# Kernel tuning notes

Hardware: AMD Instinct MI355X
Metric: run time of the kernel (lower is better)

The kernel has to match this reference:

```python
import jax, jax.numpy as jnp
import numpy as np

H = 256
LATENT = 128
NODE_FEATS = (12, 5, 4)
EDGE_FEATS = (5, 4)
END_NODE = NODE_FEATS[0] - 1
MAX_NODES = 64


def setup_inputs() -> dict:
    key = jax.random.key(0)
    ks = iter(jax.random.split(key, 40))
    def rn(shape, s=0.1):
        return jax.random.normal(next(ks), shape, dtype=jnp.float32) * s
    inp = {
        "z": jax.random.normal(next(ks), (1, LATENT), dtype=jnp.float32),
        "lp_w": rn((H, LATENT)), "lp_b": rn((H,)),
        "nWih": rn((3 * H, H)), "nWhh": rn((3 * H, H)), "nbih": rn((3 * H,)), "nbhh": rn((3 * H,)),
        "eWih": rn((3 * H, H)), "eWhh": rn((3 * H, H)), "ebih": rn((3 * H,)), "ebhh": rn((3 * H,)),
    }
    for j, f in enumerate(NODE_FEATS):
        inp[f"nc{j}_w"] = rn((f, H)); inp[f"nc{j}_b"] = rn((f,))
    for j, f in enumerate(EDGE_FEATS):
        inp[f"ec{j}_w"] = rn((f, H)); inp[f"ec{j}_b"] = rn((f,))
    inp["max_nodes"] = MAX_NODES
    return inp


def _gru(x, h, Wih, Whh, bih, bhh):
    # torch.nn.GRU single step, single layer. x,h: (1,H)
    gi = x @ Wih.T + bih
    gh = h @ Whh.T + bhh
    ir, iz, inn = jnp.split(gi, 3, axis=-1)
    hr, hz, hn = jnp.split(gh, 3, axis=-1)
    r = jax.nn.sigmoid(ir + hr)
    zg = jax.nn.sigmoid(iz + hz)
    n = jnp.tanh(inn + r * hn)
    return (1.0 - zg) * n + zg * h


def _classify(emb, W, b):
    # Linear -> softmax -> (max prob, argmax), batch=1 -> scalars
    p = jax.nn.softmax(emb @ W.T + b, axis=-1)[0]
    return jnp.max(p), jnp.argmax(p)


def _generate(z, lp_w, lp_b, nWih, nWhh, nbih, nbhh, eWih, eWhh, ebih, ebhh,
              nc0_w, nc0_b, nc1_w, nc1_b, nc2_w, nc2_b,
              ec0_w, ec0_b, ec1_w, ec1_b, max_nodes):
    node_cls = ((nc0_w, nc0_b), (nc1_w, nc1_b), (nc2_w, nc2_b))
    edge_cls = ((ec0_w, ec0_b), (ec1_w, ec1_b))
    h0 = z @ lp_w.T + lp_b                     # latent_project; set_context
    buf0 = jnp.zeros((max_nodes, 1, H), z.dtype)  # node embedding history

    def step(carry, i):
        h, buf, done = carry
        x = jnp.where(i == 0, jnp.zeros((1, H), z.dtype), buf[jnp.maximum(i - 1, 0)])
        h1 = _gru(x, h, nWih, nWhh, nbih, nbhh)   # node_celli.forward_unit; emb = h1
        nps, nis = zip(*[_classify(h1, W, b) for W, b in node_cls])
        nprobs = jnp.stack(nps)                   # (3,)
        nidxs = jnp.stack(nis)                    # (3,) int
        is_end = nidxs[0] == END_NODE

        # edge cell: seq over previous node embeddings, most recent first
        def estep(he, t):
            valid = t < i
            src = jnp.clip(i - 1 - t, 0, max_nodes - 1)
            he2 = _gru(buf[src], he, eWih, eWhh, ebih, ebhh)
            he_new = jnp.where(valid, he2, he)
            eps, eis = zip(*[_classify(he_new, W, b) for W, b in edge_cls])
            return he_new, (jnp.stack(eps), jnp.stack(eis))

        he_fin, (ep_t, ei_t) = jax.lax.scan(estep, h1, jnp.arange(max_nodes))
        # reindex: edge for source node j was produced at inner step t = i-1-j
        js = jnp.arange(max_nodes)
        ts = jnp.clip(i - 1 - js, 0, max_nodes - 1)
        ep_row = ep_t[ts]                          # (max_nodes, 2)
        ei_row = ei_t[ts]
        vj = js < i
        no_edges = jnp.all(jnp.where(vj, ei_row[:, 0] == 0, True)) & (i > 0)

        active = jnp.logical_not(done)
        node_ok = active & jnp.logical_not(is_end) & jnp.logical_not(no_edges)
        done_new = done | is_end | no_edges

        h_next = jnp.where(node_ok & (i > 0), he_fin, h1)  # node hidden <- edge hidden
        h_next = jnp.where(active, h_next, h)
        buf_new = buf.at[i].set(jnp.where(node_ok, h1, buf[i]))

        edge_valid = vj & node_ok & (i > 0)
        out = (jnp.where(node_ok, nprobs, 0.0), nidxs, node_ok,
               jnp.where(edge_valid[:, None], ep_row, 0.0), ei_row, edge_valid)
        return (h_next, buf_new, done_new), out

    _, outs = jax.lax.scan(step, (h0, buf0, jnp.zeros((), bool)), jnp.arange(max_nodes))
    # node_probs (M,3), node_idxs (M,3), node_valid (M,),
    # edge_probs (M,M,2), edge_idxs (M,M,2), edge_valid (M,M)
    return outs


def reference(z, lp_w, lp_b, nWih, nWhh, nbih, nbhh, eWih, eWhh, ebih, ebhh,
              nc0_w, nc0_b, nc1_w, nc1_b, nc2_w, nc2_b,
              ec0_w, ec0_b, ec1_w, ec1_b, max_nodes):
    return _generate(z, lp_w, lp_b, nWih, nWhh, nbih, nbhh, eWih, eWhh, ebih, ebhh,
                     nc0_w, nc0_b, nc1_w, nc1_b, nc2_w, nc2_b,
                     ec0_w, ec0_b, ec1_w, ec1_b, max_nodes)
```

## Files before the change

### kernel.cpp

```cpp
#include <hip/hip_runtime.h>
#include <stdint.h>


#define H 256
#define HL 128
#define G3 768
#define NW 16
#define SL 16
#define MAXN 64
#define NSTATE (1 + MAXN + (MAXN*(MAXN-1))/2)
#define SENTU 0xFFFFFFFFu
#define PAD 264

#define WG_CLS NW
#define WG_HELP0 (NW+1)
#define NHELP_PER 6
#define NROLE (WG_HELP0 + 2*NHELP_PER)
#define NWG 256

#define NP_OFF 0
#define NI_OFF 192
#define NV_OFF 384
#define EP_OFF 448
#define EI_OFF (EP_OFF + MAXN*MAXN*2)
#define EV_OFF (EI_OFF + MAXN*MAXN*2)

struct Wksp {
  float h[NSTATE][H];
  float gi_e[MAXN][G3];
  float gi_n[MAXN][G3];
  unsigned int dec[MAXN];
};

union Shm {
  struct {
    float whe[3*SL*PAD];
    float whn[3*SL*PAD];
    float hcur[2][H];
    float bihe[3*SL], bhhe[3*SL], bihn[3*SL], bhhn[3*SL];
    float zv[HL];
    unsigned int dec;
  } w;
  struct {
    float cw[30*H];
    float cb[30];
    float hc[H];
    float logits[30];
    float resp[5];
    int   resi[5];
    float ept[MAXN][2];
    int   eit[MAXN][2];
  } c;
  struct { float h1[H]; } hp;
};

__device__ __forceinline__ float spinf(const float* p) {
  const unsigned int* u = (const unsigned int*)p;
  unsigned int v = __hip_atomic_load(u, __ATOMIC_RELAXED, __HIP_MEMORY_SCOPE_AGENT);
  while (v == SENTU)
    v = __hip_atomic_load(u, __ATOMIC_RELAXED, __HIP_MEMORY_SCOPE_AGENT);
  return __uint_as_float(v);
}
__device__ __forceinline__ void pubf(float* p, float x) {
  __hip_atomic_store((unsigned int*)p, __float_as_uint(x),
                     __ATOMIC_RELAXED, __HIP_MEMORY_SCOPE_AGENT);
}
__device__ __forceinline__ unsigned int spinu(const unsigned int* p) {
  unsigned int v = __hip_atomic_load(p, __ATOMIC_RELAXED, __HIP_MEMORY_SCOPE_AGENT);
  while (v == SENTU)
    v = __hip_atomic_load(p, __ATOMIC_RELAXED, __HIP_MEMORY_SCOPE_AGENT);
  return v;
}
__device__ __forceinline__ void pubu(unsigned int* p, unsigned int x) {
  __hip_atomic_store(p, x, __ATOMIC_RELAXED, __HIP_MEMORY_SCOPE_AGENT);
}
__device__ __forceinline__ float sigm(float x) { return 1.0f / (1.0f + expf(-x)); }

__global__ __launch_bounds__(256)
void Generator_34746285425383_kernel(
    const float* __restrict__ z, const float* __restrict__ lp_w, const float* __restrict__ lp_b,
    const float* __restrict__ nWih, const float* __restrict__ nWhh,
    const float* __restrict__ nbih, const float* __restrict__ nbhh,
    const float* __restrict__ eWih, const float* __restrict__ eWhh,
    const float* __restrict__ ebih, const float* __restrict__ ebhh,
    const float* __restrict__ nc0w, const float* __restrict__ nc0b,
    const float* __restrict__ nc1w, const float* __restrict__ nc1b,
    const float* __restrict__ nc2w, const float* __restrict__ nc2b,
    const float* __restrict__ ec0w, const float* __restrict__ ec0b,
    const float* __restrict__ ec1w, const float* __restrict__ ec1b,
    float* __restrict__ out, Wksp* __restrict__ ws)
{
  __shared__ Shm S;
  const int bid = blockIdx.x;
  const int tid = threadIdx.x;

  if (bid < NW) {
    const int w = bid, g = tid >> 4, c = tid & 15;
    const int k = w * SL + g;
    for (int r = 0; r < 3 * SL; ++r) {
      const int gate = r / SL, gg = r % SL;
      const int grow = gate * H + (w * SL + gg);
      for (int col = tid; col < H; col += 256) {
        S.w.whe[r * PAD + col] = eWhh[grow * H + col];
        S.w.whn[r * PAD + col] = nWhh[grow * H + col];
      }
    }
    if (tid < 3 * SL) {
      const int gate = tid / SL, gg = tid % SL;
      const int grow = gate * H + w * SL + gg;
      S.w.bihe[tid] = ebih[grow]; S.w.bhhe[tid] = ebhh[grow];
      S.w.bihn[tid] = nbih[grow]; S.w.bhhn[tid] = nbhh[grow];
    }
    if (tid < HL) S.w.zv[tid] = z[tid];
    __syncthreads();

    {
      float p = 0.f;
      for (int it = 0; it < 8; ++it) {
        const int col = c + 16 * it;
        p += S.w.zv[col] * lp_w[k * HL + col];
      }
      for (int off = 1; off < 16; off <<= 1) p += __shfl_xor(p, off);
      if (c == 0) pubf(&ws->h[0][k], p + lp_b[k]);
    }

    int m = 1, idx_carry = 0;
    bool done = false;
    unsigned long long valid = 0ull;
    float pg0 = 0.f, pg1 = 0.f, pg2 = 0.f;
    const float* pga = nullptr;

    for (int i = 0; i < MAXN; ++i) {
      for (int t = -1; t < i; ++t) {
        const bool is_node = (t < 0);
        const int hidx = is_node ? idx_carry : (m - 1);
        const int src  = is_node ? (i - 1) : (i - 1 - t);
        float* hc = S.w.hcur[m & 1];
        hc[tid] = spinf(&ws->h[hidx][tid]);
        float gi0 = 0.f, gi1 = 0.f, gi2 = 0.f;
        const bool use_gi = (src >= 0) && ((valid >> src) & 1ull);
        if (use_gi) {
          gi0 = pg0; gi1 = pg1; gi2 = pg2;
          if (__float_as_uint(gi0) == SENTU) gi0 = spinf(&pga[0 * H + k]);
          if (__float_as_uint(gi1) == SENTU) gi1 = spinf(&pga[1 * H + k]);
          if (__float_as_uint(gi2) == SENTU) gi2 = spinf(&pga[2 * H + k]);
        }
        __syncthreads();
        const float* Wl = is_node ? S.w.whn : S.w.whe;
        float p0 = 0.f, p1 = 0.f, p2 = 0.f;
        #pragma unroll
        for (int it = 0; it < 16; ++it) {
          const int col = c + 16 * it;
          const float hv = hc[col];
          p0 += Wl[(0 * SL + g) * PAD + col] * hv;
          p1 += Wl[(1 * SL + g) * PAD + col] * hv;
          p2 += Wl[(2 * SL + g) * PAD + col] * hv;
        }
        for (int off = 1; off < 16; off <<= 1) {
          p0 += __shfl_xor(p0, off);
          p1 += __shfl_xor(p1, off);
          p2 += __shfl_xor(p2, off);
        }
        const float* bih = is_node ? S.w.bihn : S.w.bihe;
        const float* bhh = is_node ? S.w.bhhn : S.w.bhhe;
        const float rr = sigm(gi0 + bih[0 * SL + g] + p0 + bhh[0 * SL + g]);
        const float zz = sigm(gi1 + bih[1 * SL + g] + p1 + bhh[1 * SL + g]);
        const float nn = tanhf(gi2 + bih[2 * SL + g] + rr * (p2 + bhh[2 * SL + g]));
        const float hp = (1.f - zz) * nn + zz * hc[k];
        if (c == 0) pubf(&ws->h[m][k], hp);
        {
          int ni = i, nt = t + 1;
          if (nt >= i) { ni = i + 1; nt = -1; }
          if (ni < MAXN) {
            const bool nnode = (nt < 0);
            const int nsrc = nnode ? (ni - 1) : (ni - 1 - nt);
            if (nsrc >= 0) {
              pga = nnode ? ws->gi_n[nsrc] : ws->gi_e[nsrc];
              pg0 = __builtin_nontemporal_load(&pga[0 * H + k]);
              pg1 = __builtin_nontemporal_load(&pga[1 * H + k]);
              pg2 = __builtin_nontemporal_load(&pga[2 * H + k]);
            }
          }
        }
        ++m;
      }
      if (tid == 0) S.w.dec = spinu(&ws->dec[i]);
      __syncthreads();
      const unsigned int dec = S.w.dec;
      const bool is_end   = (dec >> 1) & 1u;
      const bool no_edges = (dec >> 2) & 1u;
      const bool active   = !done;
      const bool node_ok  = active && !is_end && !no_edges;
      if (node_ok) valid |= (1ull << i);
      const int s_end = m - 1, node_m = m - 1 - i;
      if (active) idx_carry = (node_ok && i > 0) ? s_end : node_m;
      done = done || is_end || no_edges;
    }

  } else if (bid == WG_CLS) {
    const int g = tid >> 4, c = tid & 15;
    const float* wsrc[5] = { nc0w, nc1w, nc2w, ec0w, ec1w };
    const float* bsrc[5] = { nc0b, nc1b, nc2b, ec0b, ec1b };
    const int hbase[5] = { 0, 12, 17, 21, 26 };
    const int hlen[5]  = { 12, 5, 4, 5, 4 };
    for (int hh = 0; hh < 5; ++hh)
      for (int r = 0; r < hlen[hh]; ++r)
        for (int col = tid; col < H; col += 256)
          S.c.cw[(hbase[hh] + r) * H + col] = wsrc[hh][r * H + col];
    if (tid < 30) {
      const int hh = tid < 12 ? 0 : tid < 17 ? 1 : tid < 21 ? 2 : tid < 26 ? 3 : 4;
      S.c.cb[tid] = bsrc[hh][tid - hbase[hh]];
    }
    __syncthreads();

    int m = 1;
    bool done = false;
    for (int i = 0; i < MAXN; ++i) {
      float npmax[3]; int nidx[3];
      bool is_end = false, andacc = true;
      for (int t = -1; t < i; ++t) {
        S.c.hc[tid] = spinf(&ws->h[m][tid]);
        __syncthreads();
        for (int rsel = 0; rsel < 2; ++rsel) {
          const int r = g + 16 * rsel;
          float p = 0.f;
          if (r < 30) {
            #pragma unroll
            for (int it = 0; it < 16; ++it) {
              const int col = c + 16 * it;
              p += S.c.cw[r * H + col] * S.c.hc[col];
            }
          }
          for (int off = 1; off < 16; off <<= 1) p += __shfl_xor(p, off);
          if (r < 30 && c == 0) S.c.logits[r] = p + S.c.cb[r];
        }
        __syncthreads();
        if (tid < 5) {
          const int base = hbase[tid], len = hlen[tid];
          float best = S.c.logits[base]; int bi = 0;
          for (int j = 1; j < len; ++j) {
            const float l = S.c.logits[base + j];
            if (l > best) { best = l; bi = j; }
          }
          float s = 0.f;
          for (int j = 0; j < len; ++j) s += expf(S.c.logits[base + j] - best);
          S.c.resp[tid] = 1.0f / s;
          S.c.resi[tid] = bi;
        }
        __syncthreads();
        if (t < 0) {
          npmax[0] = S.c.resp[0]; npmax[1] = S.c.resp[1]; npmax[2] = S.c.resp[2];
          nidx[0] = S.c.resi[0]; nidx[1] = S.c.resi[1]; nidx[2] = S.c.resi[2];
          is_end = (S.c.resi[0] == 11);
          if (i == 0 && tid == 0) {
            S.c.ept[0][0] = S.c.resp[3]; S.c.ept[0][1] = S.c.resp[4];
            S.c.eit[0][0] = S.c.resi[3]; S.c.eit[0][1] = S.c.resi[4];
          }
        } else {
          if (tid == 0) {
            S.c.ept[t][0] = S.c.resp[3]; S.c.ept[t][1] = S.c.resp[4];
            S.c.eit[t][0] = S.c.resi[3]; S.c.eit[t][1] = S.c.resi[4];
          }
          andacc = andacc && (S.c.resi[3] == 0);
        }
        __syncthreads();
        ++m;
      }
      const bool no_edges = (i > 0) && andacc;
      const bool active = !done;
      const bool node_ok = active && !is_end && !no_edges;
      if (tid == 0)
        pubu(&ws->dec[i], 1u | (is_end ? 2u : 0u) | (no_edges ? 4u : 0u));
      if (tid < MAXN) {
        const int j = tid;
        const bool vj = j < i;
        const bool ev = vj && node_ok && (i > 0);
        const int tt = vj ? (i - 1 - j) : 0;
        out[EP_OFF + (i * MAXN + j) * 2 + 0] = ev ? S.c.ept[tt][0] : 0.f;
        out[EP_OFF + (i * MAXN + j) * 2 + 1] = ev ? S.c.ept[tt][1] : 0.f;
        out[EI_OFF + (i * MAXN + j) * 2 + 0] = (float)S.c.eit[tt][0];
        out[EI_OFF + (i * MAXN + j) * 2 + 1] = (float)S.c.eit[tt][1];
        out[EV_OFF + i * MAXN + j] = ev ? 1.f : 0.f;
      } else if (tid < MAXN + 8) {
        const int q = tid - MAXN;
        if (q < 3)       out[NP_OFF + i * 3 + q]       = node_ok ? npmax[q] : 0.f;
        else if (q < 6)  out[NI_OFF + i * 3 + (q - 3)] = (float)nidx[q - 3];
        else if (q == 6) out[NV_OFF + i]               = node_ok ? 1.f : 0.f;
      }
      done = done || is_end || no_edges;
      __syncthreads();
    }

  } else if (bid < NROLE) {
    const int e = bid - WG_HELP0;
    const bool is_edge = (e < NHELP_PER);
    const int rowbase = (e % NHELP_PER) * 128;
    const float* Wih = is_edge ? eWih : nWih;
    float* gdst = is_edge ? &ws->gi_e[0][0] : &ws->gi_n[0][0];
    const int g = tid >> 4, c = tid & 15;
    int m_node = 1;
    for (int i = 0; i < MAXN; ++i) {
      S.hp.h1[tid] = spinf(&ws->h[m_node][tid]);
      __syncthreads();
      for (int rr = 0; rr < 8; ++rr) {
        const int row = rowbase + g * 8 + rr;
        float p = 0.f;
        #pragma unroll
        for (int u = 0; u < 4; ++u) {
          const float4 wv = *(const float4*)&Wih[row * H + c * 16 + u * 4];
          p += wv.x * S.hp.h1[c * 16 + u * 4 + 0]
             + wv.y * S.hp.h1[c * 16 + u * 4 + 1]
             + wv.z * S.hp.h1[c * 16 + u * 4 + 2]
             + wv.w * S.hp.h1[c * 16 + u * 4 + 3];
        }
        for (int off = 1; off < 16; off <<= 1) p += __shfl_xor(p, off);
        if (c == 0) pubf(&gdst[i * G3 + row], p);
      }
      __syncthreads();
      m_node += 1 + i;
    }

  } else {
    const unsigned int* flag = &ws->dec[MAXN - 1];
    float acc = (float)tid * 0.001f;
    const float bb = 1.0000001f, aa = 0.5f;
    for (;;) {
      unsigned int v = __hip_atomic_load(flag, __ATOMIC_RELAXED, __HIP_MEMORY_SCOPE_AGENT);
      if (v != SENTU) break;
      #pragma unroll 8
      for (int it = 0; it < 512; ++it) acc = __builtin_fmaf(acc, bb, aa);
    }
    asm volatile("" :: "v"(acc));
  }
}

extern "C" void kernel_launch(void* const* d_in, const int* in_sizes, int n_in,
                              void* d_out, int out_size, void* d_ws, size_t ws_size,
                              hipStream_t stream) {
  hipMemsetAsync(d_ws, 0xFF, sizeof(Wksp), stream);
  Generator_34746285425383_kernel<<<dim3(NWG), dim3(256), 0, stream>>>(
      (const float*)d_in[0],  (const float*)d_in[1],  (const float*)d_in[2],
      (const float*)d_in[3],  (const float*)d_in[4],  (const float*)d_in[5],
      (const float*)d_in[6],  (const float*)d_in[7],  (const float*)d_in[8],
      (const float*)d_in[9],  (const float*)d_in[10],
      (const float*)d_in[11], (const float*)d_in[12],
      (const float*)d_in[13], (const float*)d_in[14],
      (const float*)d_in[15], (const float*)d_in[16],
      (const float*)d_in[17], (const float*)d_in[18],
      (const float*)d_in[19], (const float*)d_in[20],
      (float*)d_out, (Wksp*)d_ws);
}
```

Baseline: 5.079 ms.

## Co-locate all pipeline roles on one XCC and poll via L2-coherent sc0 loads

Each workgroup reads its XCC id and takes a per-XCC ticket. The first XCC to gather enough workgroups for every role becomes the winner, and roles are handed out only to workgroups on that XCC, so all cross-workgroup flag and data exchange stays within one XCD's L2. Publishes and polls add sc0 global loads and stores, with a bounded retry before falling back to agent-scope atomics. The spare spinning heater workgroups are removed, and a timeout path falls back to the original blockIdx-based role assignment. This adds a startup election, an extra memset, and reliance on per-XCC cache coherence behaviour.

```diff
diff --git a/kernel.cpp b/kernel.cpp
--- a/kernel.cpp
+++ b/kernel.cpp
@@ -1,5 +1,6 @@
 #include <hip/hip_runtime.h>
 #include <stdint.h>
+#include <cstddef>
 
 
 #define H 256
@@ -10,6 +11,7 @@
 #define MAXN 64
 #define NSTATE (1 + MAXN + (MAXN*(MAXN-1))/2)
 #define SENTU 0xFFFFFFFFu
+#define DEADV 0x0000DEADu
 #define PAD 264
 
 #define WG_CLS NW
@@ -30,6 +32,9 @@
   float gi_e[MAXN][G3];
   float gi_n[MAXN][G3];
   unsigned int dec[MAXN];
+  unsigned int winner;
+  unsigned int padw[7];
+  unsigned int ticket[8];
 };
 
 union Shm {
@@ -54,25 +59,37 @@
   struct { float h1[H]; } hp;
 };
 
-__device__ __forceinline__ float spinf(const float* p) {
-  const unsigned int* u = (const unsigned int*)p;
-  unsigned int v = __hip_atomic_load(u, __ATOMIC_RELAXED, __HIP_MEMORY_SCOPE_AGENT);
-  while (v == SENTU)
-    v = __hip_atomic_load(u, __ATOMIC_RELAXED, __HIP_MEMORY_SCOPE_AGENT);
-  return __uint_as_float(v);
+__device__ __forceinline__ unsigned int ld_sc0(const unsigned int* p) {
+  unsigned int v;
+  asm volatile("global_load_dword %0, %1, off sc0\n\ts_waitcnt vmcnt(0)"
+               : "=&v"(v) : "v"(p) : "memory");
+  return v;
+}
+__device__ __forceinline__ void st_sc0(unsigned int* p, unsigned int v) {
+  asm volatile("global_store_dword %0, %1, off sc0" :: "v"(p), "v"(v) : "memory");
+}
+__device__ __forceinline__ unsigned int ld_ag(const unsigned int* p) {
+  return __hip_atomic_load(p, __ATOMIC_RELAXED, __HIP_MEMORY_SCOPE_AGENT);
+}
+__device__ __forceinline__ void pub_u(unsigned int* p, unsigned int v) {
+  __hip_atomic_store(p, v, __ATOMIC_RELAXED, __HIP_MEMORY_SCOPE_AGENT);
+  st_sc0(p, v);
 }
 __device__ __forceinline__ void pubf(float* p, float x) {
-  __hip_atomic_store((unsigned int*)p, __float_as_uint(x),
-                     __ATOMIC_RELAXED, __HIP_MEMORY_SCOPE_AGENT);
-}
-__device__ __forceinline__ unsigned int spinu(const unsigned int* p) {
-  unsigned int v = __hip_atomic_load(p, __ATOMIC_RELAXED, __HIP_MEMORY_SCOPE_AGENT);
-  while (v == SENTU)
-    v = __hip_atomic_load(p, __ATOMIC_RELAXED, __HIP_MEMORY_SCOPE_AGENT);
+  pub_u((unsigned int*)p, __float_as_uint(x));
+}
+__device__ __forceinline__ unsigned int spin_u(const unsigned int* p, bool sc) {
+  unsigned int v;
+  if (sc) {
+    int tries = 0;
+    v = ld_sc0(p);
+    while (v == SENTU && ++tries < 8) v = ld_sc0(p);
+  } else v = ld_ag(p);
+  while (v == SENTU) v = ld_ag(p);
   return v;
 }
-__device__ __forceinline__ void pubu(unsigned int* p, unsigned int x) {
-  __hip_atomic_store(p, x, __ATOMIC_RELAXED, __HIP_MEMORY_SCOPE_AGENT);
+__device__ __forceinline__ float spinf(const float* p, bool sc) {
+  return __uint_as_float(spin_u((const unsigned int*)p, sc));
 }
 __device__ __forceinline__ float sigm(float x) { return 1.0f / (1.0f + expf(-x)); }
 
@@ -91,8 +108,43 @@
     float* __restrict__ out, Wksp* __restrict__ ws)
 {
   __shared__ Shm S;
-  const int bid = blockIdx.x;
+  __shared__ int role_s, mode_s;
   const int tid = threadIdx.x;
+
+  if (tid == 0) {
+    unsigned int xcc;
+    asm volatile("s_getreg_b32 %0, hwreg(HW_REG_XCC_ID)" : "=s"(xcc));
+    xcc &= 7u;
+    const unsigned int slot = __hip_atomic_fetch_add(&ws->ticket[xcc], 1u,
+                                __ATOMIC_RELAXED, __HIP_MEMORY_SCOPE_AGENT);
+    if (slot == NROLE - 1) {
+      unsigned int exp = SENTU;
+      __hip_atomic_compare_exchange_strong(&ws->winner, &exp, xcc,
+          __ATOMIC_RELAXED, __ATOMIC_RELAXED, __HIP_MEMORY_SCOPE_AGENT);
+    }
+    unsigned int wv = ld_ag(&ws->winner);
+    int iters = 0;
+    while (wv == SENTU) {
+      ++iters;
+      if (iters > 1500 && blockIdx.x == 0) {
+        unsigned int exp = SENTU;
+        __hip_atomic_compare_exchange_strong(&ws->winner, &exp, DEADV,
+            __ATOMIC_RELAXED, __ATOMIC_RELAXED, __HIP_MEMORY_SCOPE_AGENT);
+      }
+      wv = ld_ag(&ws->winner);
+    }
+    if (wv <= 7u) {
+      role_s = (wv == xcc && slot < NROLE) ? (int)slot : -1;
+      mode_s = 1;
+    } else {
+      role_s = ((int)blockIdx.x < NROLE) ? (int)blockIdx.x : -1;
+      mode_s = 0;
+    }
+  }
+  __syncthreads();
+  const int bid = role_s;
+  const bool sc = (mode_s != 0);
+  if (bid < 0) return;
 
   if (bid < NW) {
     const int w = bid, g = tid >> 4, c = tid & 15;
@@ -136,14 +188,14 @@
         const int hidx = is_node ? idx_carry : (m - 1);
         const int src  = is_node ? (i - 1) : (i - 1 - t);
         float* hc = S.w.hcur[m & 1];
-        hc[tid] = spinf(&ws->h[hidx][tid]);
+        hc[tid] = spinf(&ws->h[hidx][tid], sc);
         float gi0 = 0.f, gi1 = 0.f, gi2 = 0.f;
         const bool use_gi = (src >= 0) && ((valid >> src) & 1ull);
         if (use_gi) {
           gi0 = pg0; gi1 = pg1; gi2 = pg2;
-          if (__float_as_uint(gi0) == SENTU) gi0 = spinf(&pga[0 * H + k]);
-          if (__float_as_uint(gi1) == SENTU) gi1 = spinf(&pga[1 * H + k]);
-          if (__float_as_uint(gi2) == SENTU) gi2 = spinf(&pga[2 * H + k]);
+          if (__float_as_uint(gi0) == SENTU) gi0 = spinf(&pga[0 * H + k], sc);
+          if (__float_as_uint(gi1) == SENTU) gi1 = spinf(&pga[1 * H + k], sc);
+          if (__float_as_uint(gi2) == SENTU) gi2 = spinf(&pga[2 * H + k], sc);
         }
         __syncthreads();
         const float* Wl = is_node ? S.w.whn : S.w.whe;
@@ -184,7 +236,7 @@
         }
         ++m;
       }
-      if (tid == 0) S.w.dec = spinu(&ws->dec[i]);
+      if (tid == 0) S.w.dec = spin_u(&ws->dec[i], sc);
       __syncthreads();
       const unsigned int dec = S.w.dec;
       const bool is_end   = (dec >> 1) & 1u;
@@ -219,7 +271,7 @@
       float npmax[3]; int nidx[3];
       bool is_end = false, andacc = true;
       for (int t = -1; t < i; ++t) {
-        S.c.hc[tid] = spinf(&ws->h[m][tid]);
+        S.c.hc[tid] = spinf(&ws->h[m][tid], sc);
         __syncthreads();
         for (int rsel = 0; rsel < 2; ++rsel) {
           const int r = g + 16 * rsel;
@@ -270,7 +322,7 @@
       const bool active = !done;
       const bool node_ok = active && !is_end && !no_edges;
       if (tid == 0)
-        pubu(&ws->dec[i], 1u | (is_end ? 2u : 0u) | (no_edges ? 4u : 0u));
+        pub_u(&ws->dec[i], 1u | (is_end ? 2u : 0u) | (no_edges ? 4u : 0u));
       if (tid < MAXN) {
         const int j = tid;
         const bool vj = j < i;
@@ -291,7 +343,7 @@
       __syncthreads();
     }
 
-  } else if (bid < NROLE) {
+  } else {
     const int e = bid - WG_HELP0;
     const bool is_edge = (e < NHELP_PER);
     const int rowbase = (e % NHELP_PER) * 128;
@@ -300,7 +352,7 @@
     const int g = tid >> 4, c = tid & 15;
     int m_node = 1;
     for (int i = 0; i < MAXN; ++i) {
-      S.hp.h1[tid] = spinf(&ws->h[m_node][tid]);
+      S.hp.h1[tid] = spinf(&ws->h[m_node][tid], sc);
       __syncthreads();
       for (int rr = 0; rr < 8; ++rr) {
         const int row = rowbase + g * 8 + rr;
@@ -319,25 +371,15 @@
       __syncthreads();
       m_node += 1 + i;
     }
-
-  } else {
-    const unsigned int* flag = &ws->dec[MAXN - 1];
-    float acc = (float)tid * 0.001f;
-    const float bb = 1.0000001f, aa = 0.5f;
-    for (;;) {
-      unsigned int v = __hip_atomic_load(flag, __ATOMIC_RELAXED, __HIP_MEMORY_SCOPE_AGENT);
-      if (v != SENTU) break;
-      #pragma unroll 8
-      for (int it = 0; it < 512; ++it) acc = __builtin_fmaf(acc, bb, aa);
-    }
-    asm volatile("" :: "v"(acc));
   }
 }
 
 extern "C" void kernel_launch(void* const* d_in, const int* in_sizes, int n_in,
                               void* d_out, int out_size, void* d_ws, size_t ws_size,
                               hipStream_t stream) {
-  hipMemsetAsync(d_ws, 0xFF, sizeof(Wksp), stream);
+  hipMemsetAsync(d_ws, 0xFF, offsetof(Wksp, ticket), stream);
+  hipMemsetAsync((char*)d_ws + offsetof(Wksp, ticket), 0,
+                 sizeof(Wksp) - offsetof(Wksp, ticket), stream);
   Generator_34746285425383_kernel<<<dim3(NWG), dim3(256), 0, stream>>>(
       (const float*)d_in[0],  (const float*)d_in[1],  (const float*)d_in[2],
       (const float*)d_in[3],  (const float*)d_in[4],  (const float*)d_in[5],
```

After: 8.296 ms. 1.63x slower.
